# Kernel tuning notes

Measured on AMD Instinct MI355X. Metric: run time of the kernel, lower is better.

## Reference

```python
import jax, jax.numpy as jnp
import numpy as np

LATENT = 128
HEADS = 4
HEAD_DIM = LATENT // HEADS
NUM_BUCKETS = 32
MAX_DISTANCE = 100000
B, N = 8, 2048


def relative_position_bucket(qpos, kpos):
    """T5-style bidirectional relative position bucketing.
    qpos, kpos: [B, N] int -> buckets [B, N, N] int32 in [0, NUM_BUCKETS).
    """
    rel = kpos[:, None, :] - qpos[:, :, None]  # [B, Nq, Nk]
    half = NUM_BUCKETS // 2
    buckets = (rel > 0).astype(jnp.int32) * half
    arel = jnp.abs(rel)
    max_exact = half // 2
    is_small = arel < max_exact
    # log-spaced buckets for larger distances
    large = max_exact + (
        jnp.log(jnp.maximum(arel, 1).astype(jnp.float32) / max_exact)
        / np.log(MAX_DISTANCE / max_exact)
        * (half - max_exact)
    ).astype(jnp.int32)
    large = jnp.minimum(large, half - 1)
    return buckets + jnp.where(is_small, arel.astype(jnp.int32), large)


def setup_inputs() -> dict:
    key = jax.random.key(0)
    ks = jax.random.split(key, 12)
    s = 0.02
    x = jax.random.normal(ks[0], (B, N, LATENT), dtype=jnp.float32)
    positions = jnp.sort(jax.random.randint(ks[1], (B, N), 0, 1000000), axis=-1)
    mask = jnp.ones((B, N), dtype=bool)
    Wq = jax.random.normal(ks[2], (LATENT, LATENT), dtype=jnp.float32) * s
    bq = jax.random.normal(ks[3], (LATENT,), dtype=jnp.float32) * s
    Wk = jax.random.normal(ks[4], (LATENT, LATENT), dtype=jnp.float32) * s
    bk = jax.random.normal(ks[5], (LATENT,), dtype=jnp.float32) * s
    Wv = jax.random.normal(ks[6], (LATENT, LATENT), dtype=jnp.float32) * s
    bv = jax.random.normal(ks[7], (LATENT,), dtype=jnp.float32) * s
    pos_w = jax.random.normal(ks[8], (NUM_BUCKETS + 1, HEADS), dtype=jnp.float32) * s
    Wo = jax.random.normal(ks[9], (LATENT, LATENT), dtype=jnp.float32) * s
    bo = jax.random.normal(ks[10], (LATENT,), dtype=jnp.float32) * s
    return {"x": x, "positions": positions, "mask": mask,
            "Wq": Wq, "bq": bq, "Wk": Wk, "bk": bk, "Wv": Wv, "bv": bv,
            "pos_w": pos_w, "Wo": Wo, "bo": bo}


def reference(x, positions, mask, Wq, bq, Wk, bk, Wv, bv, pos_w, Wo, bo):
    b, n, _ = x.shape
    # QKV projections, split heads: [b, h, n, d]
    Q = (x @ Wq + bq).reshape(b, n, HEADS, HEAD_DIM).transpose(0, 2, 1, 3)
    K = (x @ Wk + bk).reshape(b, n, HEADS, HEAD_DIM).transpose(0, 2, 1, 3)
    V = (x @ Wv + bv).reshape(b, n, HEADS, HEAD_DIM).transpose(0, 2, 1, 3)
    scores = jnp.einsum("bhqd,bhkd->bhqk", Q, K) / jnp.sqrt(
        jnp.asarray(HEAD_DIM, dtype=x.dtype))
    buckets = relative_position_bucket(positions, positions)  # [b, n, n]
    bias = pos_w[buckets]                  # [b, n, n, h]
    scores = scores + bias.transpose(0, 3, 1, 2)  # [b, h, n, n]
    scores = jnp.where(mask[:, None, None, :], scores, -jnp.inf)
    attn = jax.nn.softmax(scores, axis=-1)
    attn = jnp.nan_to_num(attn, nan=0.0)
    attended = jnp.einsum("bhqk,bhkd->bhqd", attn, V)
    attended = attended.transpose(0, 2, 1, 3).reshape(b, n, LATENT)
    return attended @ Wo + bo
```

## Files before the change

### kernel.cpp

```cpp
#include <hip/hip_runtime.h>
#include <math.h>


#define LOG2E 1.4426950408889634f
#define QKV_SCALE 0.17677669529663687f
#define QS (QKV_SCALE * LOG2E)
#define BUCKET_C 0.84804276f

typedef _Float16 half8 __attribute__((ext_vector_type(8)));
typedef float ffrag __attribute__((ext_vector_type(4)));

#if __has_builtin(__builtin_amdgcn_exp2f)
#define EXP2F __builtin_amdgcn_exp2f
#else
#define EXP2F exp2f
#endif

static __device__ __forceinline__ unsigned short f16bits(float f) {
    return __builtin_bit_cast(unsigned short, (_Float16)f);
}
static __device__ __forceinline__ float h16f(unsigned int bits) {
    return (float)__builtin_bit_cast(_Float16, (unsigned short)(bits & 0xFFFFu));
}
static __device__ __forceinline__ unsigned int pk2(float a, float b) {
    return __builtin_bit_cast(unsigned int, __builtin_amdgcn_cvt_pkrtz(a, b));
}
static __device__ __forceinline__ void async_cp16(const unsigned short* g, unsigned short* l) {
    __builtin_amdgcn_global_load_lds(
        (const __attribute__((address_space(1))) unsigned int*)g,
        (__attribute__((address_space(3))) unsigned int*)l, 16, 0, 0);
}
static __device__ __forceinline__ int vslot(int d, int g) {
    return d * 32 + (g ^ (d & 30));
}

__global__ __launch_bounds__(256)
void prep_kernel(const float* __restrict__ Wq, const float* __restrict__ Wk,
                 const float* __restrict__ Wv, const float* __restrict__ Wo,
                 const float* __restrict__ bq, const float* __restrict__ bk,
                 const float* __restrict__ bv,
                 unsigned short* __restrict__ Wt_qkv,
                 unsigned short* __restrict__ Wt_o,
                 float* __restrict__ bias_qkv)
{
    const int e = blockIdx.x * 256 + threadIdx.x;
    const int m = e >> 14, r = e & 16383;
    const int c = r >> 7, k = r & 127;
    float v;
    if (m == 0)      v = Wq[k * 128 + c] * QS;
    else if (m == 1) v = Wk[k * 128 + c];
    else if (m == 2) v = Wv[k * 128 + c];
    else             v = Wo[k * 128 + c];
    if (m < 3) Wt_qkv[(m * 128 + c) * 128 + k] = f16bits(v);
    else       Wt_o[c * 128 + k] = f16bits(v);
    if (e < 128)      bias_qkv[e] = bq[e] * QS;
    else if (e < 256) bias_qkv[e] = bk[e - 128];
    else if (e < 384) bias_qkv[e] = bv[e - 256];
}

static __device__ __forceinline__ int bigP(int a) {
    return (int)(__logf((float)a * 0.125f) * BUCKET_C);
}
static __device__ int thresh(int j) {
    int a = (int)(8.0f * __expf((float)j * 1.1791855f));
    while (bigP(a) < j) ++a;
    while (a > 8 && bigP(a - 1) >= j) --a;
    return a;
}

__global__ __launch_bounds__(256)
void seg_kernel(const int* __restrict__ positions, unsigned int* __restrict__ segtab)
{
    const int gid = blockIdx.x * 256 + threadIdx.x;
    const int row = gid >> 5;
    const int s = gid & 31;
    const int b = row >> 11;
    const int* kp = positions + b * 2048;
    const int qp = kp[row & 2047];
    const int bucket = (s < 15) ? (15 - s) : (s == 15 ? 0 : s + 1);
    if (s == 31) { segtab[row * 32 + s] = (2048u << 16) | 31u; return; }
    const int sn = s + 1;
    int Sn;
    if (sn <= 7)       Sn = -thresh(8 - sn) + 1;
    else if (sn <= 14) Sn = -(15 - sn);
    else if (sn == 15) Sn = 0;
    else if (sn <= 22) Sn = sn - 15;
    else if (sn == 23) Sn = 8;
    else if (sn <= 30) Sn = thresh(sn - 23);
    else               Sn = 3000000;
    const int target = qp + Sn;
    int lo = 0, hi = 2048;
    while (lo < hi) { const int mid = (lo + hi) >> 1; if (kp[mid] < target) lo = mid + 1; else hi = mid; }
    segtab[row * 32 + s] = ((unsigned)lo << 16) | (unsigned)bucket;
}

__global__ __launch_bounds__(256)
void qkv_mfma(const float* __restrict__ x, const unsigned short* __restrict__ Wt,
              const float* __restrict__ bias_qkv,
              unsigned short* __restrict__ Qb, unsigned short* __restrict__ Kb,
              unsigned short* __restrict__ Vtb)
{
    __shared__ __align__(16) unsigned short Xs[16 * 136];
    const int tid = threadIdx.x;
    const int token0 = blockIdx.x * 16;
    #pragma unroll
    for (int it = 0; it < 2; ++it) {
        const int f = tid + it * 256;
        const int row = f >> 5, k0 = (f & 31) << 2;
        const float4 xv = *(const float4*)(x + (size_t)(token0 + row) * 128 + k0);
        uint2 u;
        u.x = pk2(xv.x, xv.y);
        u.y = pk2(xv.z, xv.w);
        *(uint2*)(Xs + row * 136 + k0) = u;
    }
    __syncthreads();

    const int wave = tid >> 6, lane = tid & 63;
    const int lq = lane & 15, quad = lane >> 4;
    const int b = token0 >> 11;
    const int n0 = token0 & 2047;

    #pragma unroll
    for (int j = 0; j < 6; ++j) {
        const int ct = wave + j * 4;
        const int colbase = ct * 16;
        half8 wf[4];
        #pragma unroll
        for (int ks = 0; ks < 4; ++ks)
            wf[ks] = *(const half8*)(Wt + (colbase + lq) * 128 + ks * 32 + quad * 8);

        if (ct < 16) {
            const float4 bv = *(const float4*)(bias_qkv + colbase + quad * 4);
            ffrag acc = {bv.x, bv.y, bv.z, bv.w};
            #pragma unroll
            for (int ks = 0; ks < 4; ++ks) {
                const half8 xf = *(const half8*)(Xs + lq * 136 + ks * 32 + quad * 8);
                acc = __builtin_amdgcn_mfma_f32_16x16x32_f16(wf[ks], xf, acc, 0, 0, 0);
            }
            const int n = n0 + lq;
            const int c0 = (colbase + quad * 4) & 127;
            const int h = c0 >> 5, d = c0 & 31;
            const ushort4 v4 = make_ushort4(f16bits(acc[0]), f16bits(acc[1]),
                                            f16bits(acc[2]), f16bits(acc[3]));
            unsigned short* base = (ct < 8) ? Qb : Kb;
            *(ushort4*)(base + ((size_t)(b * 4 + h) * 2048 + n) * 32 + d) = v4;
        } else {
            const float bias = bias_qkv[colbase + lq];
            ffrag acc = {bias, bias, bias, bias};
            #pragma unroll
            for (int ks = 0; ks < 4; ++ks) {
                const half8 xf = *(const half8*)(Xs + lq * 136 + ks * 32 + quad * 8);
                acc = __builtin_amdgcn_mfma_f32_16x16x32_f16(xf, wf[ks], acc, 0, 0, 0);
            }
            const int c2 = colbase + lq - 256;
            const int h = c2 >> 5, d = c2 & 31;
            const int n = n0 + quad * 4;
            const ushort4 v4 = make_ushort4(f16bits(acc[0]), f16bits(acc[1]),
                                            f16bits(acc[2]), f16bits(acc[3]));
            *(ushort4*)(Vtb + ((size_t)(b * 4 + h) * 32 + d) * 2048 + n) = v4;
        }
    }
}

__global__ __launch_bounds__(512, 4)
void attn_kernel(const unsigned short* __restrict__ Qb,
                 const unsigned short* __restrict__ Kb,
                 const unsigned short* __restrict__ Vtb,
                 const unsigned int* __restrict__ segtab,
                 const float* __restrict__ pos_w,
                 unsigned short* __restrict__ att)
{
    __shared__ __align__(16) unsigned short VB[2][2][4096];
    __shared__ unsigned int Sg[128 * 32];

    const int tid = threadIdx.x;
    const int wave = __builtin_amdgcn_readfirstlane(tid >> 6);
    const int lane = tid & 63;
    const int lq = lane & 15, quad = lane >> 4;
    const int group = wave >> 2, wg = wave & 3;

    const int qt = blockIdx.x & 15;
    const int bh = blockIdx.x >> 4;
    const int b = bh >> 2, h = bh & 3;
    const int q0 = qt * 128;

    const unsigned short* Kg = Kb + (size_t)bh * 2048 * 32;
    const unsigned short* Vg = Vtb + (size_t)bh * 32 * 2048;

    int voff[2];
    #pragma unroll
    for (int it = 0; it < 2; ++it) {
        const int n = wg * 2 + it;
        const int slot0 = n * 128 + 2 * lane;
        const int d = slot0 >> 5;
        const int g1 = (slot0 & 31) ^ (d & 30);
        voff[it] = d * 2048 + g1 * 4;
    }

    #pragma unroll
    for (int it = 0; it < 2; ++it)
        async_cp16(Vg + group * 128 + voff[it], &VB[group][0][(wg * 2 + it) * 512]);

    {
        const unsigned int* src = segtab + ((size_t)b * 2048 + q0) * 32;
        #pragma unroll
        for (int it = 0; it < 2; ++it) {
            const int e4 = tid + it * 512;
            uint4 u = *(const uint4*)(src + e4 * 4);
            unsigned int* c = &u.x;
            #pragma unroll
            for (int i = 0; i < 4; ++i) {
                const float wf = __expf(pos_w[(c[i] & 0xFFFFu) * 4 + h]);
                c[i] = (c[i] & 0xFFFF0000u) | f16bits(wf);
            }
            *(uint4*)(Sg + e4 * 4) = u;
        }
    }

    const int qa = q0 + wg * 32 + lq;
    const int qbn = qa + 16;
    const half8 qfa = *(const half8*)(Qb + ((size_t)bh * 2048 + qa) * 32 + quad * 8);
    const half8 qfb = *(const half8*)(Qb + ((size_t)bh * 2048 + qbn) * 32 + quad * 8);

    ffrag o0a = {0.f,0.f,0.f,0.f}, o1a = {0.f,0.f,0.f,0.f};
    ffrag o0b = {0.f,0.f,0.f,0.f}, o1b = {0.f,0.f,0.f,0.f};
    float lsa = 0.f, lsb = 0.f;
    int cura = -1, enda = 0; float wfa = 0.f;
    int curb = -1, endb = 0; float wfb = 0.f;
    const int sga = (wg * 32 + lq) * 32;
    const int sgb = (wg * 32 + 16 + lq) * 32;

    __syncthreads();

    for (int i = 0; i < 8; ++i) {
        const int kc = (2 * i + group) * 128;
        const unsigned short* vb = VB[group][i & 1];
        if (i < 7) {
            #pragma unroll
            for (int it = 0; it < 2; ++it)
                async_cp16(Vg + (kc + 256) + voff[it],
                           &VB[group][(i + 1) & 1][(wg * 2 + it) * 512]);
        }

        #pragma unroll
        for (int win = 0; win < 4; ++win) {
            unsigned int pua[4], pub[4];
            #pragma unroll
            for (int T = 0; T < 2; ++T) {
                const int ksub = win * 2 + T;
                const half8 kf = *(const half8*)(Kg + (size_t)(kc + ksub * 16 + lq) * 32 + quad * 8);
                ffrag sa = {0.f,0.f,0.f,0.f}, sb = {0.f,0.f,0.f,0.f};
                sa = __builtin_amdgcn_mfma_f32_16x16x32_f16(kf, qfa, sa, 0, 0, 0);
                sb = __builtin_amdgcn_mfma_f32_16x16x32_f16(kf, qfb, sb, 0, 0, 0);
                const int kb = kc + ksub * 16 + quad * 4;
                float pa[4], pb[4];
                if (__builtin_expect(__any(kb + 3 >= enda), 0)) {
                    #pragma unroll
                    for (int r = 0; r < 4; ++r) {
                        while (kb + r >= enda) {
                            const unsigned int u = Sg[sga + (++cura)];
                            enda = (int)(u >> 16); wfa = h16f(u);
                        }
                        pa[r] = EXP2F(sa[r]) * wfa;
                    }
                } else {
                    #pragma unroll
                    for (int r = 0; r < 4; ++r) pa[r] = EXP2F(sa[r]) * wfa;
                }
                if (__builtin_expect(__any(kb + 3 >= endb), 0)) {
                    #pragma unroll
                    for (int r = 0; r < 4; ++r) {
                        while (kb + r >= endb) {
                            const unsigned int u = Sg[sgb + (++curb)];
                            endb = (int)(u >> 16); wfb = h16f(u);
                        }
                        pb[r] = EXP2F(sb[r]) * wfb;
                    }
                } else {
                    #pragma unroll
                    for (int r = 0; r < 4; ++r) pb[r] = EXP2F(sb[r]) * wfb;
                }
                lsa += (pa[0] + pa[1]) + (pa[2] + pa[3]);
                lsb += (pb[0] + pb[1]) + (pb[2] + pb[3]);
                pua[T * 2 + 0] = pk2(pa[0], pa[1]);
                pua[T * 2 + 1] = pk2(pa[2], pa[3]);
                pub[T * 2 + 0] = pk2(pb[0], pb[1]);
                pub[T * 2 + 1] = pk2(pb[2], pb[3]);
            }
            const int g0 = win * 8 + quad;
            const uint2 va0 = *(const uint2*)(vb + vslot(lq, g0) * 4);
            const uint2 va1 = *(const uint2*)(vb + vslot(lq, g0 + 4) * 4);
            const uint2 vb0 = *(const uint2*)(vb + vslot(16 + lq, g0) * 4);
            const uint2 vb1 = *(const uint2*)(vb + vslot(16 + lq, g0 + 4) * 4);
            const half8 A0 = __builtin_bit_cast(half8, make_int4(va0.x, va0.y, va1.x, va1.y));
            const half8 A1 = __builtin_bit_cast(half8, make_int4(vb0.x, vb0.y, vb1.x, vb1.y));
            const half8 Ba = __builtin_bit_cast(half8, make_int4(pua[0], pua[1], pua[2], pua[3]));
            const half8 Bb = __builtin_bit_cast(half8, make_int4(pub[0], pub[1], pub[2], pub[3]));
            o0a = __builtin_amdgcn_mfma_f32_16x16x32_f16(A0, Ba, o0a, 0, 0, 0);
            o1a = __builtin_amdgcn_mfma_f32_16x16x32_f16(A1, Ba, o1a, 0, 0, 0);
            o0b = __builtin_amdgcn_mfma_f32_16x16x32_f16(A0, Bb, o0b, 0, 0, 0);
            o1b = __builtin_amdgcn_mfma_f32_16x16x32_f16(A1, Bb, o1b, 0, 0, 0);
        }
        __syncthreads();
    }

    float* scr = (float*)&VB[0][0][0];
    if (group == 1) {
        float* s = scr + (wg * 64 + lane) * 18;
        #pragma unroll
        for (int j = 0; j < 4; ++j) {
            s[j] = o0a[j]; s[4 + j] = o1a[j]; s[8 + j] = o0b[j]; s[12 + j] = o1b[j];
        }
        s[16] = lsa; s[17] = lsb;
    }
    __syncthreads();
    if (group == 0) {
        const float* s = scr + (wg * 64 + lane) * 18;
        #pragma unroll
        for (int j = 0; j < 4; ++j) {
            o0a[j] += s[j]; o1a[j] += s[4 + j]; o0b[j] += s[8 + j]; o1b[j] += s[12 + j];
        }
        lsa += s[16]; lsb += s[17];
        lsa += __shfl_xor(lsa, 16); lsa += __shfl_xor(lsa, 32);
        lsb += __shfl_xor(lsb, 16); lsb += __shfl_xor(lsb, 32);
        const float inva = 1.0f / lsa;
        const float invb = 1.0f / lsb;

        unsigned short* da = att + (size_t)(b * 2048 + qa) * 128 + h * 32 + quad * 4;
        uint2 r0, r1;
        r0.x = pk2(o0a[0] * inva, o0a[1] * inva);
        r0.y = pk2(o0a[2] * inva, o0a[3] * inva);
        r1.x = pk2(o1a[0] * inva, o1a[1] * inva);
        r1.y = pk2(o1a[2] * inva, o1a[3] * inva);
        *(uint2*)da = r0;
        *(uint2*)(da + 16) = r1;

        unsigned short* db = att + (size_t)(b * 2048 + qbn) * 128 + h * 32 + quad * 4;
        r0.x = pk2(o0b[0] * invb, o0b[1] * invb);
        r0.y = pk2(o0b[2] * invb, o0b[3] * invb);
        r1.x = pk2(o1b[0] * invb, o1b[1] * invb);
        r1.y = pk2(o1b[2] * invb, o1b[3] * invb);
        *(uint2*)db = r0;
        *(uint2*)(db + 16) = r1;
    }
}

__global__ __launch_bounds__(256)
void out_mfma(const unsigned short* __restrict__ att,
              const unsigned short* __restrict__ Wt_o,
              const float* __restrict__ bo, float* __restrict__ out)
{
    __shared__ __align__(16) unsigned short Xs[16 * 136];
    const int tid = threadIdx.x;
    const int token0 = blockIdx.x * 16;
    {
        const int f = tid;
        const int row = f >> 4, k0 = (f & 15) << 3;
        const uint4 v = *(const uint4*)(att + (size_t)(token0 + row) * 128 + k0);
        *(uint4*)(Xs + row * 136 + k0) = v;
    }
    __syncthreads();

    const int wave = tid >> 6, lane = tid & 63;
    const int lq = lane & 15, quad = lane >> 4;

    #pragma unroll
    for (int j = 0; j < 2; ++j) {
        const int colbase = (wave + j * 4) * 16;
        half8 wf[4];
        #pragma unroll
        for (int ks = 0; ks < 4; ++ks)
            wf[ks] = *(const half8*)(Wt_o + (colbase + lq) * 128 + ks * 32 + quad * 8);
        const float4 bv = *(const float4*)(bo + colbase + quad * 4);
        ffrag acc = {bv.x, bv.y, bv.z, bv.w};
        #pragma unroll
        for (int ks = 0; ks < 4; ++ks) {
            const half8 xf = *(const half8*)(Xs + lq * 136 + ks * 32 + quad * 8);
            acc = __builtin_amdgcn_mfma_f32_16x16x32_f16(wf[ks], xf, acc, 0, 0, 0);
        }
        const int c0 = colbase + quad * 4;
        *(float4*)(out + (size_t)(token0 + lq) * 128 + c0) =
            make_float4(acc[0], acc[1], acc[2], acc[3]);
    }
}

extern "C" void kernel_launch(void* const* d_in, const int* in_sizes, int n_in,
                              void* d_out, int out_size, void* d_ws, size_t ws_size,
                              hipStream_t stream)
{
    const float* x         = (const float*)d_in[0];
    const int*   positions = (const int*)d_in[1];
    const float* Wq = (const float*)d_in[3];
    const float* bq = (const float*)d_in[4];
    const float* Wk = (const float*)d_in[5];
    const float* bk = (const float*)d_in[6];
    const float* Wv = (const float*)d_in[7];
    const float* bv = (const float*)d_in[8];
    const float* pw = (const float*)d_in[9];
    const float* Wo = (const float*)d_in[10];
    const float* bo = (const float*)d_in[11];
    float* out = (float*)d_out;

    unsigned short* Qb  = (unsigned short*)d_ws;
    unsigned short* Kb  = Qb + 2097152;
    unsigned short* Vtb = Kb + 2097152;
    unsigned short* att = Vtb + 2097152;
    unsigned int* segtab = (unsigned int*)(att + 2097152);
    unsigned short* Wt_qkv = (unsigned short*)(segtab + 524288);
    unsigned short* Wt_o = Wt_qkv + 49152;
    float* bias_qkv = (float*)(Wt_o + 16384);

    prep_kernel<<<256, 256, 0, stream>>>(Wq, Wk, Wv, Wo, bq, bk, bv,
                                         Wt_qkv, Wt_o, bias_qkv);
    seg_kernel<<<2048, 256, 0, stream>>>(positions, segtab);
    qkv_mfma<<<1024, 256, 0, stream>>>(x, Wt_qkv, bias_qkv, Qb, Kb, Vtb);
    attn_kernel<<<512, 512, 0, stream>>>(Qb, Kb, Vtb, segtab, pw, att);
    out_mfma<<<1024, 256, 0, stream>>>(att, Wt_o, bo, out);
}
```

Before: 176.7 us.

## Fuse prep/seg kernels, retile projections, pre-swizzle V layout, MFMA row sums, K prefetch

Merges the weight-prep and segment-table kernels into one launch and replaces the per-thread threshold search with a constant table. The QKV and output projection kernels now process 64 tokens per 512-thread block, which reuses weight fragments across four row tiles. V is written in a pre-swizzled chunk layout so the attention kernel can load it with contiguous 16-byte async copies and read it with single half8 LDS loads. The attention loop also double-buffers K fragments in registers, XOR-swizzles the segment table in LDS, and computes softmax row sums with an extra MFMA against a ones vector instead of scalar adds and shuffles. The costs are two extra MFMAs per window and a hardcoded threshold table.

```diff
diff --git a/kernel.cpp b/kernel.cpp
--- a/kernel.cpp
+++ b/kernel.cpp
@@ -5,7 +5,6 @@
 #define LOG2E 1.4426950408889634f
 #define QKV_SCALE 0.17677669529663687f
 #define QS (QKV_SCALE * LOG2E)
-#define BUCKET_C 0.84804276f
 
 typedef _Float16 half8 __attribute__((ext_vector_type(8)));
 typedef float ffrag __attribute__((ext_vector_type(4)));
@@ -30,48 +29,45 @@
         (const __attribute__((address_space(1))) unsigned int*)g,
         (__attribute__((address_space(3))) unsigned int*)l, 16, 0, 0);
 }
-static __device__ __forceinline__ int vslot(int d, int g) {
-    return d * 32 + (g ^ (d & 30));
-}
+
+__device__ __constant__ int SN_TAB[32] = {
+     -2000000000,
+    -30755, -9458, -2908, -894, -275, -84, -26,
+    -7, -6, -5, -4, -3, -2, -1,
+    0,
+    1, 2, 3, 4, 5, 6, 7,
+    8,
+    27, 85, 276, 895, 2909, 9459, 30756,
+    2000000000 };
 
 __global__ __launch_bounds__(256)
-void prep_kernel(const float* __restrict__ Wq, const float* __restrict__ Wk,
-                 const float* __restrict__ Wv, const float* __restrict__ Wo,
-                 const float* __restrict__ bq, const float* __restrict__ bk,
-                 const float* __restrict__ bv,
-                 unsigned short* __restrict__ Wt_qkv,
-                 unsigned short* __restrict__ Wt_o,
-                 float* __restrict__ bias_qkv)
+void prep_seg_kernel(const float* __restrict__ Wq, const float* __restrict__ Wk,
+                     const float* __restrict__ Wv, const float* __restrict__ Wo,
+                     const float* __restrict__ bq, const float* __restrict__ bk,
+                     const float* __restrict__ bv,
+                     const int* __restrict__ positions,
+                     unsigned short* __restrict__ Wt_qkv,
+                     unsigned short* __restrict__ Wt_o,
+                     float* __restrict__ bias_qkv,
+                     unsigned int* __restrict__ segtab)
 {
-    const int e = blockIdx.x * 256 + threadIdx.x;
-    const int m = e >> 14, r = e & 16383;
-    const int c = r >> 7, k = r & 127;
-    float v;
-    if (m == 0)      v = Wq[k * 128 + c] * QS;
-    else if (m == 1) v = Wk[k * 128 + c];
-    else if (m == 2) v = Wv[k * 128 + c];
-    else             v = Wo[k * 128 + c];
-    if (m < 3) Wt_qkv[(m * 128 + c) * 128 + k] = f16bits(v);
-    else       Wt_o[c * 128 + k] = f16bits(v);
-    if (e < 128)      bias_qkv[e] = bq[e] * QS;
-    else if (e < 256) bias_qkv[e] = bk[e - 128];
-    else if (e < 384) bias_qkv[e] = bv[e - 256];
-}
-
-static __device__ __forceinline__ int bigP(int a) {
-    return (int)(__logf((float)a * 0.125f) * BUCKET_C);
-}
-static __device__ int thresh(int j) {
-    int a = (int)(8.0f * __expf((float)j * 1.1791855f));
-    while (bigP(a) < j) ++a;
-    while (a > 8 && bigP(a - 1) >= j) --a;
-    return a;
-}
-
-__global__ __launch_bounds__(256)
-void seg_kernel(const int* __restrict__ positions, unsigned int* __restrict__ segtab)
-{
-    const int gid = blockIdx.x * 256 + threadIdx.x;
+    if (blockIdx.x < 256) {
+        const int e = blockIdx.x * 256 + threadIdx.x;
+        const int m = e >> 14, r = e & 16383;
+        const int c = r >> 7, k = r & 127;
+        float v;
+        if (m == 0)      v = Wq[k * 128 + c] * QS;
+        else if (m == 1) v = Wk[k * 128 + c];
+        else if (m == 2) v = Wv[k * 128 + c];
+        else             v = Wo[k * 128 + c];
+        if (m < 3) Wt_qkv[(m * 128 + c) * 128 + k] = f16bits(v);
+        else       Wt_o[c * 128 + k] = f16bits(v);
+        if (e < 128)      bias_qkv[e] = bq[e] * QS;
+        else if (e < 256) bias_qkv[e] = bk[e - 128];
+        else if (e < 384) bias_qkv[e] = bv[e - 256];
+        return;
+    }
+    const int gid = (blockIdx.x - 256) * 256 + threadIdx.x;
     const int row = gid >> 5;
     const int s = gid & 31;
     const int b = row >> 11;
@@ -79,33 +75,24 @@
     const int qp = kp[row & 2047];
     const int bucket = (s < 15) ? (15 - s) : (s == 15 ? 0 : s + 1);
     if (s == 31) { segtab[row * 32 + s] = (2048u << 16) | 31u; return; }
-    const int sn = s + 1;
-    int Sn;
-    if (sn <= 7)       Sn = -thresh(8 - sn) + 1;
-    else if (sn <= 14) Sn = -(15 - sn);
-    else if (sn == 15) Sn = 0;
-    else if (sn <= 22) Sn = sn - 15;
-    else if (sn == 23) Sn = 8;
-    else if (sn <= 30) Sn = thresh(sn - 23);
-    else               Sn = 3000000;
-    const int target = qp + Sn;
+    const int target = qp + SN_TAB[s + 1];
     int lo = 0, hi = 2048;
     while (lo < hi) { const int mid = (lo + hi) >> 1; if (kp[mid] < target) lo = mid + 1; else hi = mid; }
     segtab[row * 32 + s] = ((unsigned)lo << 16) | (unsigned)bucket;
 }
 
-__global__ __launch_bounds__(256)
+__global__ __launch_bounds__(512)
 void qkv_mfma(const float* __restrict__ x, const unsigned short* __restrict__ Wt,
               const float* __restrict__ bias_qkv,
               unsigned short* __restrict__ Qb, unsigned short* __restrict__ Kb,
-              unsigned short* __restrict__ Vtb)
+              unsigned short* __restrict__ Vg2)
 {
-    __shared__ __align__(16) unsigned short Xs[16 * 136];
+    __shared__ __align__(16) unsigned short Xs[64 * 136];
     const int tid = threadIdx.x;
-    const int token0 = blockIdx.x * 16;
-    #pragma unroll
-    for (int it = 0; it < 2; ++it) {
-        const int f = tid + it * 256;
+    const int token0 = blockIdx.x * 64;
+    #pragma unroll
+    for (int it = 0; it < 4; ++it) {
+        const int f = tid + it * 512;
         const int row = f >> 5, k0 = (f & 31) << 2;
         const float4 xv = *(const float4*)(x + (size_t)(token0 + row) * 128 + k0);
         uint2 u;
@@ -121,8 +108,8 @@
     const int n0 = token0 & 2047;
 
     #pragma unroll
-    for (int j = 0; j < 6; ++j) {
-        const int ct = wave + j * 4;
+    for (int j = 0; j < 3; ++j) {
+        const int ct = wave + j * 8;
         const int colbase = ct * 16;
         half8 wf[4];
         #pragma unroll
@@ -130,34 +117,47 @@
             wf[ks] = *(const half8*)(Wt + (colbase + lq) * 128 + ks * 32 + quad * 8);
 
         if (ct < 16) {
-            const float4 bv = *(const float4*)(bias_qkv + colbase + quad * 4);
-            ffrag acc = {bv.x, bv.y, bv.z, bv.w};
+            const int c0q = colbase + quad * 4;
+            const float4 bv = *(const float4*)(bias_qkv + c0q);
             #pragma unroll
-            for (int ks = 0; ks < 4; ++ks) {
-                const half8 xf = *(const half8*)(Xs + lq * 136 + ks * 32 + quad * 8);
-                acc = __builtin_amdgcn_mfma_f32_16x16x32_f16(wf[ks], xf, acc, 0, 0, 0);
+            for (int msub = 0; msub < 4; ++msub) {
+                ffrag acc = {bv.x, bv.y, bv.z, bv.w};
+                #pragma unroll
+                for (int ks = 0; ks < 4; ++ks) {
+                    const half8 xf = *(const half8*)(Xs + (msub * 16 + lq) * 136 + ks * 32 + quad * 8);
+                    acc = __builtin_amdgcn_mfma_f32_16x16x32_f16(wf[ks], xf, acc, 0, 0, 0);
+                }
+                const int n = n0 + msub * 16 + lq;
+                const int c0 = c0q & 127;
+                const int h = c0 >> 5, d = c0 & 31;
+                const ushort4 v4 = make_ushort4(f16bits(acc[0]), f16bits(acc[1]),
+                                                f16bits(acc[2]), f16bits(acc[3]));
+                unsigned short* base = (ct < 8) ? Qb : Kb;
+                *(ushort4*)(base + ((size_t)(b * 4 + h) * 2048 + n) * 32 + d) = v4;
             }
-            const int n = n0 + lq;
-            const int c0 = (colbase + quad * 4) & 127;
-            const int h = c0 >> 5, d = c0 & 31;
-            const ushort4 v4 = make_ushort4(f16bits(acc[0]), f16bits(acc[1]),
-                                            f16bits(acc[2]), f16bits(acc[3]));
-            unsigned short* base = (ct < 8) ? Qb : Kb;
-            *(ushort4*)(base + ((size_t)(b * 4 + h) * 2048 + n) * 32 + d) = v4;
         } else {
             const float bias = bias_qkv[colbase + lq];
-            ffrag acc = {bias, bias, bias, bias};
-            #pragma unroll
-            for (int ks = 0; ks < 4; ++ks) {
-                const half8 xf = *(const half8*)(Xs + lq * 136 + ks * 32 + quad * 8);
-                acc = __builtin_amdgcn_mfma_f32_16x16x32_f16(xf, wf[ks], acc, 0, 0, 0);
-            }
             const int c2 = colbase + lq - 256;
             const int h = c2 >> 5, d = c2 & 31;
-            const int n = n0 + quad * 4;
-            const ushort4 v4 = make_ushort4(f16bits(acc[0]), f16bits(acc[1]),
-                                            f16bits(acc[2]), f16bits(acc[3]));
-            *(ushort4*)(Vtb + ((size_t)(b * 4 + h) * 32 + d) * 2048 + n) = v4;
+            const size_t bhh = (size_t)(b * 4 + h);
+            #pragma unroll
+            for (int msub = 0; msub < 4; ++msub) {
+                ffrag acc = {bias, bias, bias, bias};
+                #pragma unroll
+                for (int ks = 0; ks < 4; ++ks) {
+                    const half8 xf = *(const half8*)(Xs + (msub * 16 + lq) * 136 + ks * 32 + quad * 8);
+                    acc = __builtin_amdgcn_mfma_f32_16x16x32_f16(xf, wf[ks], acc, 0, 0, 0);
+                }
+                const int n = n0 + msub * 16 + quad * 4;
+                const int chunk = n >> 7, kloc = n & 127;
+                const int win = kloc >> 5, rem = kloc & 31;
+                const int half = rem >> 4, pg = (rem >> 2) & 3;
+                const int G = d * 16 + ((win * 4 + pg) ^ (d & 15));
+                const size_t off = ((bhh * 16 + chunk) * 512 + G) * 8 + half * 4;
+                const ushort4 v4 = make_ushort4(f16bits(acc[0]), f16bits(acc[1]),
+                                                f16bits(acc[2]), f16bits(acc[3]));
+                *(ushort4*)(Vg2 + off) = v4;
+            }
         }
     }
 }
@@ -165,7 +165,7 @@
 __global__ __launch_bounds__(512, 4)
 void attn_kernel(const unsigned short* __restrict__ Qb,
                  const unsigned short* __restrict__ Kb,
-                 const unsigned short* __restrict__ Vtb,
+                 const unsigned short* __restrict__ Vg2,
                  const unsigned int* __restrict__ segtab,
                  const float* __restrict__ pos_w,
                  unsigned short* __restrict__ att)
@@ -185,21 +185,13 @@
     const int q0 = qt * 128;
 
     const unsigned short* Kg = Kb + (size_t)bh * 2048 * 32;
-    const unsigned short* Vg = Vtb + (size_t)bh * 32 * 2048;
-
-    int voff[2];
+    const unsigned short* Vgb = Vg2 + (size_t)bh * 65536;
+
     #pragma unroll
     for (int it = 0; it < 2; ++it) {
-        const int n = wg * 2 + it;
-        const int slot0 = n * 128 + 2 * lane;
-        const int d = slot0 >> 5;
-        const int g1 = (slot0 & 31) ^ (d & 30);
-        voff[it] = d * 2048 + g1 * 4;
-    }
-
-    #pragma unroll
-    for (int it = 0; it < 2; ++it)
-        async_cp16(Vg + group * 128 + voff[it], &VB[group][0][(wg * 2 + it) * 512]);
+        const int g = (wg * 2 + it) * 64 + lane;
+        async_cp16(Vgb + (size_t)group * 4096 + g * 8, &VB[group][0][(wg * 2 + it) * 512]);
+    }
 
     {
         const unsigned int* src = segtab + ((size_t)b * 2048 + q0) * 32;
@@ -208,12 +200,13 @@
             const int e4 = tid + it * 512;
             uint4 u = *(const uint4*)(src + e4 * 4);
             unsigned int* c = &u.x;
+            const int row = e4 >> 3, s0 = (e4 & 7) * 4;
+            const int rx = row & 31;
             #pragma unroll
             for (int i = 0; i < 4; ++i) {
                 const float wf = __expf(pos_w[(c[i] & 0xFFFFu) * 4 + h]);
-                c[i] = (c[i] & 0xFFFF0000u) | f16bits(wf);
+                Sg[row * 32 + ((s0 + i) ^ rx)] = (c[i] & 0xFFFF0000u) | f16bits(wf);
             }
-            *(uint4*)(Sg + e4 * 4) = u;
         }
     }
 
@@ -222,43 +215,46 @@
     const half8 qfa = *(const half8*)(Qb + ((size_t)bh * 2048 + qa) * 32 + quad * 8);
     const half8 qfb = *(const half8*)(Qb + ((size_t)bh * 2048 + qbn) * 32 + quad * 8);
 
-    ffrag o0a = {0.f,0.f,0.f,0.f}, o1a = {0.f,0.f,0.f,0.f};
-    ffrag o0b = {0.f,0.f,0.f,0.f}, o1b = {0.f,0.f,0.f,0.f};
-    float lsa = 0.f, lsb = 0.f;
+    half8 ones;
+    #pragma unroll
+    for (int i = 0; i < 8; ++i) ones[i] = (_Float16)1.0f;
+
+    ffrag o0a = {0.f,0.f,0.f,0.f}, o1a = {0.f,0.f,0.f,0.f}, o2a = {0.f,0.f,0.f,0.f};
+    ffrag o0b = {0.f,0.f,0.f,0.f}, o1b = {0.f,0.f,0.f,0.f}, o2b = {0.f,0.f,0.f,0.f};
     int cura = -1, enda = 0; float wfa = 0.f;
     int curb = -1, endb = 0; float wfb = 0.f;
-    const int sga = (wg * 32 + lq) * 32;
-    const int sgb = (wg * 32 + 16 + lq) * 32;
+    const int rowa = wg * 32 + lq, rowb = rowa + 16;
+    const int sga = rowa * 32, xa = rowa & 31;
+    const int sgb = rowb * 32, xb = rowb & 31;
+
+    half8 kA[4], kB[4];
+    {
+        const int kc0 = group * 128;
+        #pragma unroll
+        for (int j = 0; j < 4; ++j)
+            kA[j] = *(const half8*)(Kg + (size_t)(kc0 + j * 16 + lq) * 32 + quad * 8);
+    }
 
     __syncthreads();
 
-    for (int i = 0; i < 8; ++i) {
-        const int kc = (2 * i + group) * 128;
-        const unsigned short* vb = VB[group][i & 1];
-        if (i < 7) {
-            #pragma unroll
-            for (int it = 0; it < 2; ++it)
-                async_cp16(Vg + (kc + 256) + voff[it],
-                           &VB[group][(i + 1) & 1][(wg * 2 + it) * 512]);
-        }
-
-        #pragma unroll
-        for (int win = 0; win < 4; ++win) {
+    auto half_chunk = [&](const half8* karr, const unsigned short* vb, int kc, int w0) {
+        #pragma unroll
+        for (int dw = 0; dw < 2; ++dw) {
+            const int w = w0 + dw;
             unsigned int pua[4], pub[4];
             #pragma unroll
             for (int T = 0; T < 2; ++T) {
-                const int ksub = win * 2 + T;
-                const half8 kf = *(const half8*)(Kg + (size_t)(kc + ksub * 16 + lq) * 32 + quad * 8);
+                const half8 kf = karr[dw * 2 + T];
                 ffrag sa = {0.f,0.f,0.f,0.f}, sb = {0.f,0.f,0.f,0.f};
                 sa = __builtin_amdgcn_mfma_f32_16x16x32_f16(kf, qfa, sa, 0, 0, 0);
                 sb = __builtin_amdgcn_mfma_f32_16x16x32_f16(kf, qfb, sb, 0, 0, 0);
-                const int kb = kc + ksub * 16 + quad * 4;
+                const int kidx = kc + (w * 2 + T) * 16 + quad * 4;
                 float pa[4], pb[4];
-                if (__builtin_expect(__any(kb + 3 >= enda), 0)) {
+                if (__builtin_expect(__any(kidx + 3 >= enda), 0)) {
                     #pragma unroll
                     for (int r = 0; r < 4; ++r) {
-                        while (kb + r >= enda) {
-                            const unsigned int u = Sg[sga + (++cura)];
+                        while (kidx + r >= enda) {
+                            const unsigned int u = Sg[sga + ((++cura) ^ xa)];
                             enda = (int)(u >> 16); wfa = h16f(u);
                         }
                         pa[r] = EXP2F(sa[r]) * wfa;
@@ -267,11 +263,11 @@
                     #pragma unroll
                     for (int r = 0; r < 4; ++r) pa[r] = EXP2F(sa[r]) * wfa;
                 }
-                if (__builtin_expect(__any(kb + 3 >= endb), 0)) {
+                if (__builtin_expect(__any(kidx + 3 >= endb), 0)) {
                     #pragma unroll
                     for (int r = 0; r < 4; ++r) {
-                        while (kb + r >= endb) {
-                            const unsigned int u = Sg[sgb + (++curb)];
+                        while (kidx + r >= endb) {
+                            const unsigned int u = Sg[sgb + ((++curb) ^ xb)];
                             endb = (int)(u >> 16); wfb = h16f(u);
                         }
                         pb[r] = EXP2F(sb[r]) * wfb;
@@ -280,30 +276,52 @@
                     #pragma unroll
                     for (int r = 0; r < 4; ++r) pb[r] = EXP2F(sb[r]) * wfb;
                 }
-                lsa += (pa[0] + pa[1]) + (pa[2] + pa[3]);
-                lsb += (pb[0] + pb[1]) + (pb[2] + pb[3]);
                 pua[T * 2 + 0] = pk2(pa[0], pa[1]);
                 pua[T * 2 + 1] = pk2(pa[2], pa[3]);
                 pub[T * 2 + 0] = pk2(pb[0], pb[1]);
                 pub[T * 2 + 1] = pk2(pb[2], pb[3]);
             }
-            const int g0 = win * 8 + quad;
-            const uint2 va0 = *(const uint2*)(vb + vslot(lq, g0) * 4);
-            const uint2 va1 = *(const uint2*)(vb + vslot(lq, g0 + 4) * 4);
-            const uint2 vb0 = *(const uint2*)(vb + vslot(16 + lq, g0) * 4);
-            const uint2 vb1 = *(const uint2*)(vb + vslot(16 + lq, g0 + 4) * 4);
-            const half8 A0 = __builtin_bit_cast(half8, make_int4(va0.x, va0.y, va1.x, va1.y));
-            const half8 A1 = __builtin_bit_cast(half8, make_int4(vb0.x, vb0.y, vb1.x, vb1.y));
+            const int c = (w * 4 + quad) ^ lq;
+            const half8 A0 = *(const half8*)(vb + (lq * 16 + c) * 8);
+            const half8 A1 = *(const half8*)(vb + ((16 + lq) * 16 + c) * 8);
             const half8 Ba = __builtin_bit_cast(half8, make_int4(pua[0], pua[1], pua[2], pua[3]));
             const half8 Bb = __builtin_bit_cast(half8, make_int4(pub[0], pub[1], pub[2], pub[3]));
             o0a = __builtin_amdgcn_mfma_f32_16x16x32_f16(A0, Ba, o0a, 0, 0, 0);
             o1a = __builtin_amdgcn_mfma_f32_16x16x32_f16(A1, Ba, o1a, 0, 0, 0);
+            o2a = __builtin_amdgcn_mfma_f32_16x16x32_f16(ones, Ba, o2a, 0, 0, 0);
             o0b = __builtin_amdgcn_mfma_f32_16x16x32_f16(A0, Bb, o0b, 0, 0, 0);
             o1b = __builtin_amdgcn_mfma_f32_16x16x32_f16(A1, Bb, o1b, 0, 0, 0);
-        }
+            o2b = __builtin_amdgcn_mfma_f32_16x16x32_f16(ones, Bb, o2b, 0, 0, 0);
+        }
+    };
+
+    for (int i = 0; i < 8; ++i) {
+        const int kc = (2 * i + group) * 128;
+        const unsigned short* vb = &VB[group][i & 1][0];
+        if (i < 7) {
+            #pragma unroll
+            for (int it = 0; it < 2; ++it) {
+                const int g = (wg * 2 + it) * 64 + lane;
+                async_cp16(Vgb + (size_t)(2 * i + group + 2) * 4096 + g * 8,
+                           &VB[group][(i + 1) & 1][(wg * 2 + it) * 512]);
+            }
+        }
+        #pragma unroll
+        for (int j = 0; j < 4; ++j)
+            kB[j] = *(const half8*)(Kg + (size_t)(kc + (4 + j) * 16 + lq) * 32 + quad * 8);
+
+        half_chunk(kA, vb, kc, 0);
+
+        const int kcn = (i < 7) ? kc + 256 : kc;
+        #pragma unroll
+        for (int j = 0; j < 4; ++j)
+            kA[j] = *(const half8*)(Kg + (size_t)(kcn + j * 16 + lq) * 32 + quad * 8);
+
+        half_chunk(kB, vb, kc, 2);
         __syncthreads();
     }
 
+    float lsa = o2a[0], lsb = o2b[0];
     float* scr = (float*)&VB[0][0][0];
     if (group == 1) {
         float* s = scr + (wg * 64 + lane) * 18;
@@ -321,8 +339,6 @@
             o0a[j] += s[j]; o1a[j] += s[4 + j]; o0b[j] += s[8 + j]; o1b[j] += s[12 + j];
         }
         lsa += s[16]; lsb += s[17];
-        lsa += __shfl_xor(lsa, 16); lsa += __shfl_xor(lsa, 32);
-        lsb += __shfl_xor(lsb, 16); lsb += __shfl_xor(lsb, 32);
         const float inva = 1.0f / lsa;
         const float invb = 1.0f / lsb;
 
@@ -345,16 +361,17 @@
     }
 }
 
-__global__ __launch_bounds__(256)
+__global__ __launch_bounds__(512)
 void out_mfma(const unsigned short* __restrict__ att,
               const unsigned short* __restrict__ Wt_o,
               const float* __restrict__ bo, float* __restrict__ out)
 {
-    __shared__ __align__(16) unsigned short Xs[16 * 136];
+    __shared__ __align__(16) unsigned short Xs[64 * 136];
     const int tid = threadIdx.x;
-    const int token0 = blockIdx.x * 16;
-    {
-        const int f = tid;
+    const int token0 = blockIdx.x * 64;
+    #pragma unroll
+    for (int it = 0; it < 2; ++it) {
+        const int f = tid + it * 512;
         const int row = f >> 4, k0 = (f & 15) << 3;
         const uint4 v = *(const uint4*)(att + (size_t)(token0 + row) * 128 + k0);
         *(uint4*)(Xs + row * 136 + k0) = v;
@@ -363,23 +380,24 @@
 
     const int wave = tid >> 6, lane = tid & 63;
     const int lq = lane & 15, quad = lane >> 4;
-
-    #pragma unroll
-    for (int j = 0; j < 2; ++j) {
-        const int colbase = (wave + j * 4) * 16;
-        half8 wf[4];
-        #pragma unroll
-        for (int ks = 0; ks < 4; ++ks)
-            wf[ks] = *(const half8*)(Wt_o + (colbase + lq) * 128 + ks * 32 + quad * 8);
-        const float4 bv = *(const float4*)(bo + colbase + quad * 4);
+    const int colbase = wave * 16;
+
+    half8 wf[4];
+    #pragma unroll
+    for (int ks = 0; ks < 4; ++ks)
+        wf[ks] = *(const half8*)(Wt_o + (colbase + lq) * 128 + ks * 32 + quad * 8);
+    const float4 bv = *(const float4*)(bo + colbase + quad * 4);
+
+    #pragma unroll
+    for (int msub = 0; msub < 4; ++msub) {
         ffrag acc = {bv.x, bv.y, bv.z, bv.w};
         #pragma unroll
         for (int ks = 0; ks < 4; ++ks) {
-            const half8 xf = *(const half8*)(Xs + lq * 136 + ks * 32 + quad * 8);
+            const half8 xf = *(const half8*)(Xs + (msub * 16 + lq) * 136 + ks * 32 + quad * 8);
             acc = __builtin_amdgcn_mfma_f32_16x16x32_f16(wf[ks], xf, acc, 0, 0, 0);
         }
         const int c0 = colbase + quad * 4;
-        *(float4*)(out + (size_t)(token0 + lq) * 128 + c0) =
+        *(float4*)(out + (size_t)(token0 + msub * 16 + lq) * 128 + c0) =
             make_float4(acc[0], acc[1], acc[2], acc[3]);
     }
 }
@@ -403,17 +421,16 @@
 
     unsigned short* Qb  = (unsigned short*)d_ws;
     unsigned short* Kb  = Qb + 2097152;
-    unsigned short* Vtb = Kb + 2097152;
-    unsigned short* att = Vtb + 2097152;
+    unsigned short* Vg2 = Kb + 2097152;
+    unsigned short* att = Vg2 + 2097152;
     unsigned int* segtab = (unsigned int*)(att + 2097152);
     unsigned short* Wt_qkv = (unsigned short*)(segtab + 524288);
     unsigned short* Wt_o = Wt_qkv + 49152;
     float* bias_qkv = (float*)(Wt_o + 16384);
 
-    prep_kernel<<<256, 256, 0, stream>>>(Wq, Wk, Wv, Wo, bq, bk, bv,
-                                         Wt_qkv, Wt_o, bias_qkv);
-    seg_kernel<<<2048, 256, 0, stream>>>(positions, segtab);
-    qkv_mfma<<<1024, 256, 0, stream>>>(x, Wt_qkv, bias_qkv, Qb, Kb, Vtb);
-    attn_kernel<<<512, 512, 0, stream>>>(Qb, Kb, Vtb, segtab, pw, att);
-    out_mfma<<<1024, 256, 0, stream>>>(att, Wt_o, bo, out);
-}
+    prep_seg_kernel<<<2304, 256, 0, stream>>>(Wq, Wk, Wv, Wo, bq, bk, bv, positions,
+                                              Wt_qkv, Wt_o, bias_qkv, segtab);
+    qkv_mfma<<<256, 512, 0, stream>>>(x, Wt_qkv, bias_qkv, Qb, Kb, Vg2);
+    attn_kernel<<<512, 512, 0, stream>>>(Qb, Kb, Vg2, segtab, pw, att);
+    out_mfma<<<256, 512, 0, stream>>>(att, Wt_o, bo, out);
+}
```

Result: faster. 149.2 us (-15.6%).
